# Kernel optimization log

Hardware: AMD Instinct MI355X
Metric: run time of the kernel (lower is better)

Reference implementation:

```python
import jax, jax.numpy as jnp
import numpy as np

B, S, D, H, HD = 2, 2048, 2048, 16, 128
SCALE = 1.0 / np.sqrt(HD)


def _rotate_half(x):
    x1, x2 = jnp.split(x, 2, axis=-1)
    return jnp.concatenate([-x2, x1], axis=-1)


def setup_inputs() -> dict:
    key = jax.random.key(0)
    ks = jax.random.split(key, 6)
    std = 0.02
    x = jax.random.normal(ks[0], (B, S, D), dtype=jnp.float32)
    Wq = jax.random.normal(ks[1], (D, D), dtype=jnp.float32) * std
    Wk = jax.random.normal(ks[2], (D, D), dtype=jnp.float32) * std
    Wv = jax.random.normal(ks[3], (D, D), dtype=jnp.float32) * std
    Wo = jax.random.normal(ks[4], (D, D), dtype=jnp.float32) * std
    # causal additive mask [1,1,S,S]
    neg = jnp.float32(-1e9)
    mask = jnp.where(jnp.tril(jnp.ones((S, S), dtype=bool)), 0.0, neg)[None, None]
    # standard RoPE tables [S, HD]
    inv_freq = 1.0 / (10000.0 ** (np.arange(0, HD, 2, dtype=np.float32) / HD))
    t = np.arange(S, dtype=np.float32)
    freqs = np.outer(t, inv_freq)                      # [S, HD/2]
    emb = np.concatenate([freqs, freqs], axis=-1)      # [S, HD]
    cos = jnp.asarray(np.cos(emb), dtype=jnp.float32)
    sin = jnp.asarray(np.sin(emb), dtype=jnp.float32)
    return {"x": x, "mask": mask, "cos": cos, "sin": sin,
            "Wq": Wq, "Wk": Wk, "Wv": Wv, "Wo": Wo}


def reference(x, mask, cos, sin, Wq, Wk, Wv, Wo):
    # projections (nn.Linear: y = x @ W.T)
    q = (x @ Wq.T).reshape(B, S, H, HD).transpose(0, 2, 1, 3)  # [B,H,S,HD]
    k = (x @ Wk.T).reshape(B, S, H, HD).transpose(0, 2, 1, 3)
    v = (x @ Wv.T).reshape(B, S, H, HD).transpose(0, 2, 1, 3)
    # inline RoPE
    c = cos[None, None]  # [1,1,S,HD]
    s = sin[None, None]
    q = q * c + _rotate_half(q) * s
    k = k * c + _rotate_half(k) * s
    # attention
    scores = jnp.einsum('bhqd,bhkd->bhqk', q, k) * SCALE + mask
    attn = jax.nn.softmax(scores, axis=-1)
    out = jnp.einsum('bhqk,bhkd->bhqd', attn, v)
    out = out.transpose(0, 2, 1, 3).reshape(B, S, D)
    return out @ Wo.T
```

## Files before the change

### kernel.cpp

```cpp
#include <hip/hip_runtime.h>
#include <hip/hip_bf16.h>
#include <type_traits>

#define B_  2
#define S_  2048
#define D_  2048
#define H_  16
#define HD_ 128
#define SCALE_ 0.08838834764831845f

using bf16 = __hip_bfloat16;
typedef __attribute__((ext_vector_type(8))) short short8;
typedef __attribute__((ext_vector_type(4))) short short4v;
typedef __attribute__((ext_vector_type(4))) float floatx4;

static __device__ __forceinline__ short bf16_bits(float f) {
    bf16 h = __float2bfloat16(f);
    short s;
    __builtin_memcpy(&s, &h, 2);
    return s;
}

static __device__ __forceinline__ void load_lds16(const bf16* gp, bf16* lp) {
    __builtin_amdgcn_global_load_lds(
        (const __attribute__((address_space(1))) void*)gp,
        (__attribute__((address_space(3))) void*)lp, 16, 0, 0);
}

__global__ __launch_bounds__(256) void conv_kernel(
        const float* s0, const float* s1, const float* s2,
        const float* s3, const float* s4, const float* s5,
        bf16* d0, bf16* d1, bf16* d2, bf16* d3, bf16* d4, bf16* d5) {
    int cid = blockIdx.x >> 12;
    int off = ((blockIdx.x & 4095) * 256 + threadIdx.x) * 4;
    const float* s; bf16* d;
    switch (cid) {
        case 0: s = s0; d = d0; break;
        case 1: s = s1; d = d1; break;
        case 2: s = s2; d = d2; break;
        case 3: s = s3; d = d3; break;
        case 4: s = s4; d = d4; break;
        default: s = s5; d = d5; break;
    }
    float4 f = *reinterpret_cast<const float4*>(s + off);
    short4v sv = {bf16_bits(f.x), bf16_bits(f.y), bf16_bits(f.z), bf16_bits(f.w)};
    *reinterpret_cast<short4v*>(d + off) = sv;
}

template <typename CT>
static __device__ __forceinline__ void gemm_core(const bf16* A, const bf16* W,
                                                 CT* C, int M, int N, int K,
                                                 int m0, int n0) {
    const int tid  = threadIdx.x;
    const int wave = tid >> 6;
    const int lane = tid & 63;
    const int wm = wave >> 1, wn = wave & 1;
    const int l16 = lane & 15, quad = lane >> 4;

    __shared__ __align__(16) bf16 As[128 * 32];
    __shared__ __align__(16) bf16 Bs[128 * 32];

    floatx4 acc[4][4];
    #pragma unroll
    for (int i = 0; i < 4; i++)
        #pragma unroll
        for (int j = 0; j < 4; j++)
            acc[i][j] = (floatx4){0.f, 0.f, 0.f, 0.f};

    const int srow = (lane >> 2);
    const int scol = (lane & 3) * 8;

    for (int kt = 0; kt < K; kt += 32) {
        #pragma unroll
        for (int i = 0; i < 2; i++) {
            int seg  = wave * 2 + i;
            int row  = seg * 16 + srow;
            load_lds16(&A[(size_t)(m0 + row) * K + kt + scol], &As[seg * 512]);
            load_lds16(&W[(size_t)(n0 + row) * K + kt + scol], &Bs[seg * 512]);
        }
        __syncthreads();

        short8 af[4], bfrag[4];
        #pragma unroll
        for (int m = 0; m < 4; m++)
            af[m] = *reinterpret_cast<const short8*>(&As[(wm * 64 + m * 16 + l16) * 32 + quad * 8]);
        #pragma unroll
        for (int n = 0; n < 4; n++)
            bfrag[n] = *reinterpret_cast<const short8*>(&Bs[(wn * 64 + n * 16 + l16) * 32 + quad * 8]);

        #pragma unroll
        for (int m = 0; m < 4; m++)
            #pragma unroll
            for (int n = 0; n < 4; n++)
                acc[m][n] = __builtin_amdgcn_mfma_f32_16x16x32_bf16(af[m], bfrag[n], acc[m][n], 0, 0, 0);
        __syncthreads();
    }

    #pragma unroll
    for (int m = 0; m < 4; m++) {
        #pragma unroll
        for (int n = 0; n < 4; n++) {
            #pragma unroll
            for (int r = 0; r < 4; r++) {
                int row = m0 + wm * 64 + m * 16 + quad * 4 + r;
                int col = n0 + wn * 64 + n * 16 + l16;
                if constexpr (std::is_same_v<CT, float>)
                    C[(size_t)row * N + col] = acc[m][n][r];
                else
                    C[(size_t)row * N + col] = __float2bfloat16(acc[m][n][r]);
            }
        }
    }
}

__global__ __launch_bounds__(256) void gemm_qkv(const bf16* __restrict__ X,
                                                const bf16* __restrict__ Wq,
                                                const bf16* __restrict__ Wk,
                                                const bf16* __restrict__ Wv,
                                                bf16* __restrict__ Q,
                                                bf16* __restrict__ Kb,
                                                bf16* __restrict__ V) {
    int wi = blockIdx.x >> 4;
    int n0 = (blockIdx.x & 15) * 128;
    int m0 = blockIdx.y * 128;
    const bf16* W = (wi == 0) ? Wq : (wi == 1) ? Wk : Wv;
    bf16* C = (wi == 0) ? Q : (wi == 1) ? Kb : V;
    gemm_core<bf16>(X, W, C, B_ * S_, D_, D_, m0, n0);
}

__global__ __launch_bounds__(256) void gemm_o(const bf16* __restrict__ A,
                                              const bf16* __restrict__ W,
                                              float* __restrict__ C) {
    gemm_core<float>(A, W, C, B_ * S_, D_, D_, blockIdx.y * 128, blockIdx.x * 128);
}

template <typename AT, typename CT>
__global__ __launch_bounds__(256) void gemm_bt(const AT* __restrict__ A,
                                               const float* __restrict__ W,
                                               CT* __restrict__ C,
                                               int M, int N, int K) {
    const int n0 = blockIdx.x * 128;
    const int m0 = blockIdx.y * 128;
    const int tid  = threadIdx.x;
    const int wave = tid >> 6;
    const int lane = tid & 63;
    const int wm = wave >> 1, wn = wave & 1;
    const int l16 = lane & 15, quad = lane >> 4;

    __shared__ __align__(16) bf16 As[128][40];
    __shared__ __align__(16) bf16 Bs[128][40];

    floatx4 acc[4][4];
    #pragma unroll
    for (int i = 0; i < 4; i++)
        #pragma unroll
        for (int j = 0; j < 4; j++)
            acc[i][j] = (floatx4){0.f, 0.f, 0.f, 0.f};

    for (int kt = 0; kt < K; kt += 32) {
        if constexpr (std::is_same_v<AT, float>) {
            #pragma unroll
            for (int i = 0; i < 4; i++) {
                int idx = i * 256 + tid;
                int row = idx >> 3;
                int ck  = idx & 7;
                float4 f = *reinterpret_cast<const float4*>(
                    &A[(size_t)(m0 + row) * K + kt + ck * 4]);
                short4v sv = {bf16_bits(f.x), bf16_bits(f.y),
                              bf16_bits(f.z), bf16_bits(f.w)};
                *reinterpret_cast<short4v*>(&As[row][ck * 4]) = sv;
            }
        } else {
            #pragma unroll
            for (int i = 0; i < 2; i++) {
                int idx = i * 256 + tid;
                int row = idx >> 2;
                int ck  = idx & 3;
                *reinterpret_cast<int4*>(&As[row][ck * 8]) =
                    *reinterpret_cast<const int4*>(
                        &A[(size_t)(m0 + row) * K + kt + ck * 8]);
            }
        }
        #pragma unroll
        for (int i = 0; i < 4; i++) {
            int idx = i * 256 + tid;
            int row = idx >> 3;
            int ck  = idx & 7;
            float4 f = *reinterpret_cast<const float4*>(
                &W[(size_t)(n0 + row) * K + kt + ck * 4]);
            short4v sv = {bf16_bits(f.x), bf16_bits(f.y),
                          bf16_bits(f.z), bf16_bits(f.w)};
            *reinterpret_cast<short4v*>(&Bs[row][ck * 4]) = sv;
        }
        __syncthreads();

        short8 af[4], bfrag[4];
        #pragma unroll
        for (int m = 0; m < 4; m++)
            af[m] = *reinterpret_cast<const short8*>(&As[wm * 64 + m * 16 + l16][quad * 8]);
        #pragma unroll
        for (int n = 0; n < 4; n++)
            bfrag[n] = *reinterpret_cast<const short8*>(&Bs[wn * 64 + n * 16 + l16][quad * 8]);

        #pragma unroll
        for (int m = 0; m < 4; m++)
            #pragma unroll
            for (int n = 0; n < 4; n++)
                acc[m][n] = __builtin_amdgcn_mfma_f32_16x16x32_bf16(af[m], bfrag[n], acc[m][n], 0, 0, 0);
        __syncthreads();
    }

    #pragma unroll
    for (int m = 0; m < 4; m++) {
        #pragma unroll
        for (int n = 0; n < 4; n++) {
            #pragma unroll
            for (int r = 0; r < 4; r++) {
                int row = m0 + wm * 64 + m * 16 + quad * 4 + r;
                int col = n0 + wn * 64 + n * 16 + l16;
                if constexpr (std::is_same_v<CT, float>)
                    C[(size_t)row * N + col] = acc[m][n][r];
                else
                    C[(size_t)row * N + col] = __float2bfloat16(acc[m][n][r]);
            }
        }
    }
}

__global__ __launch_bounds__(256) void rope_kernel(bf16* __restrict__ q,
                                                   bf16* __restrict__ k,
                                                   const float* __restrict__ cosT,
                                                   const float* __restrict__ sinT) {
    int idx = blockIdx.x * blockDim.x + threadIdx.x;
    int d = idx & 63;
    int h = (idx >> 6) & 15;
    int s = (idx >> 10) & 2047;
    int rest = idx >> 21;
    int b = rest & 1;
    bool isq = !(rest >> 1);
    bf16* p = isq ? q : k;
    float sc = isq ? SCALE_ : 1.0f;
    size_t base = ((size_t)(b * S_ + s)) * D_ + h * HD_;
    float v0 = __bfloat162float(p[base + d]);
    float v1 = __bfloat162float(p[base + d + 64]);
    float c0 = cosT[s * HD_ + d];
    float s0 = sinT[s * HD_ + d];
    float c1 = cosT[s * HD_ + d + 64];
    float s1 = sinT[s * HD_ + d + 64];
    p[base + d]      = __float2bfloat16((v0 * c0 - v1 * s0) * sc);
    p[base + d + 64] = __float2bfloat16((v1 * c1 + v0 * s1) * sc);
}

__global__ __launch_bounds__(256) void attn_kernel(const bf16* q,
                                                   const bf16* k,
                                                   const bf16* v,
                                                   bf16* o) {
    const int bx = blockIdx.x;
    const int qt = 15 - (bx & 15);
    const int h  = (bx >> 4) & 15;
    const int b  = bx >> 8;
    const int q0 = qt * 128;
    const int tid  = threadIdx.x;
    const int wave = tid >> 6;
    const int lane = tid & 63;
    const int l16 = lane & 15, quad = lane >> 4;

    __shared__ __align__(16) bf16  Ks[32][136];
    __shared__ __align__(16) short Vt[128][36];
    __shared__ __align__(16) short Pl[4][2][16][40];

    const size_t head_off = (size_t)b * S_ * D_ + (size_t)h * HD_;
    const bf16* qh = q + head_off;
    const bf16* kh = k + head_off;
    const short* vh = reinterpret_cast<const short*>(v) + head_off;

    short8 qf[2][4];
    #pragma unroll
    for (int mb = 0; mb < 2; mb++) {
        const bf16* qrow = qh + (size_t)(q0 + wave * 32 + mb * 16 + l16) * D_;
        #pragma unroll
        for (int dstep = 0; dstep < 4; dstep++)
            qf[mb][dstep] = *reinterpret_cast<const short8*>(qrow + dstep * 32 + quad * 8);
    }

    floatx4 ov[2][8];
    floatx4 lacc[2];
    #pragma unroll
    for (int mb = 0; mb < 2; mb++) {
        lacc[mb] = (floatx4){0.f, 0.f, 0.f, 0.f};
        #pragma unroll
        for (int i = 0; i < 8; i++) ov[mb][i] = (floatx4){0.f, 0.f, 0.f, 0.f};
    }
    float mrow[2][4];
    #pragma unroll
    for (int mb = 0; mb < 2; mb++)
        #pragma unroll
        for (int r = 0; r < 4; r++) mrow[mb][r] = -1e30f;

    const short ONEB = 0x3F80;
    const short8 ones = {ONEB, ONEB, ONEB, ONEB, ONEB, ONEB, ONEB, ONEB};

    const int vd  = tid & 127;
    const int vkh = tid >> 7;

    const int nkt = qt * 4 + 4;
    for (int kt = 0; kt < nkt; kt++) {
        const int k0 = kt * 32;
        #pragma unroll
        for (int i = 0; i < 2; i++) {
            int idx = i * 256 + tid;
            int row = idx >> 4;
            int ck  = idx & 15;
            *reinterpret_cast<int4*>(&Ks[row][ck * 8]) =
                *reinterpret_cast<const int4*>(kh + (size_t)(k0 + row) * D_ + ck * 8);
        }
        {
            const short* vcol = vh + (size_t)(k0 + vkh * 16) * D_ + vd;
            short tmp[16];
            #pragma unroll
            for (int r = 0; r < 16; r++)
                tmp[r] = vcol[(size_t)r * D_];
            #pragma unroll
            for (int c = 0; c < 4; c++) {
                short4v sv = {tmp[c*4], tmp[c*4+1], tmp[c*4+2], tmp[c*4+3]};
                *reinterpret_cast<short4v*>(&Vt[vd][vkh * 16 + c * 4]) = sv;
            }
        }
        __syncthreads();

        floatx4 sc[2][2];
        #pragma unroll
        for (int mb = 0; mb < 2; mb++)
            #pragma unroll
            for (int nb = 0; nb < 2; nb++)
                sc[mb][nb] = (floatx4){0.f, 0.f, 0.f, 0.f};
        #pragma unroll
        for (int dstep = 0; dstep < 4; dstep++) {
            short8 kf0 = *reinterpret_cast<const short8*>(&Ks[l16][dstep * 32 + quad * 8]);
            short8 kf1 = *reinterpret_cast<const short8*>(&Ks[16 + l16][dstep * 32 + quad * 8]);
            #pragma unroll
            for (int mb = 0; mb < 2; mb++) {
                sc[mb][0] = __builtin_amdgcn_mfma_f32_16x16x32_bf16(qf[mb][dstep], kf0, sc[mb][0], 0, 0, 0);
                sc[mb][1] = __builtin_amdgcn_mfma_f32_16x16x32_bf16(qf[mb][dstep], kf1, sc[mb][1], 0, 0, 0);
            }
        }

        #pragma unroll
        for (int mb = 0; mb < 2; mb++) {
            const int qbase = q0 + wave * 32 + mb * 16;
            const bool need_mask = (k0 + 31 > qbase);
            #pragma unroll
            for (int r = 0; r < 4; r++) {
                float s0 = sc[mb][0][r];
                float s1 = sc[mb][1][r];
                if (need_mask) {
                    int qg = qbase + quad * 4 + r;
                    if (k0 + l16 > qg)      s0 = -1e30f;
                    if (k0 + 16 + l16 > qg) s1 = -1e30f;
                }
                float mx = fmaxf(s0, s1);
                #pragma unroll
                for (int off = 1; off < 16; off <<= 1)
                    mx = fmaxf(mx, __shfl_xor(mx, off, 16));
                float mnew  = fmaxf(mrow[mb][r], mx);
                float alpha = __expf(mrow[mb][r] - mnew);
                mrow[mb][r] = mnew;
                Pl[wave][mb][quad * 4 + r][l16]      = bf16_bits(__expf(s0 - mnew));
                Pl[wave][mb][quad * 4 + r][16 + l16] = bf16_bits(__expf(s1 - mnew));
                lacc[mb][r] *= alpha;
                #pragma unroll
                for (int db = 0; db < 8; db++) ov[mb][db][r] *= alpha;
            }
        }

        __asm__ volatile("s_waitcnt lgkmcnt(0)" ::: "memory");

        short8 pf0 = *reinterpret_cast<const short8*>(&Pl[wave][0][l16][quad * 8]);
        short8 pf1 = *reinterpret_cast<const short8*>(&Pl[wave][1][l16][quad * 8]);
        #pragma unroll
        for (int db = 0; db < 8; db++) {
            const short* vp = &Vt[db * 16 + l16][quad * 8];
            short4v a = *reinterpret_cast<const short4v*>(vp);
            short4v c = *reinterpret_cast<const short4v*>(vp + 4);
            short8 vf = {a[0], a[1], a[2], a[3], c[0], c[1], c[2], c[3]};
            ov[0][db] = __builtin_amdgcn_mfma_f32_16x16x32_bf16(pf0, vf, ov[0][db], 0, 0, 0);
            ov[1][db] = __builtin_amdgcn_mfma_f32_16x16x32_bf16(pf1, vf, ov[1][db], 0, 0, 0);
        }
        lacc[0] = __builtin_amdgcn_mfma_f32_16x16x32_bf16(pf0, ones, lacc[0], 0, 0, 0);
        lacc[1] = __builtin_amdgcn_mfma_f32_16x16x32_bf16(pf1, ones, lacc[1], 0, 0, 0);
        __syncthreads();
    }

    bf16* oh = o + head_off;
    #pragma unroll
    for (int mb = 0; mb < 2; mb++) {
        #pragma unroll
        for (int r = 0; r < 4; r++) {
            float inv = 1.f / lacc[mb][r];
            int srow = q0 + wave * 32 + mb * 16 + quad * 4 + r;
            #pragma unroll
            for (int db = 0; db < 8; db++)
                oh[(size_t)srow * D_ + db * 16 + l16] = __float2bfloat16(ov[mb][db][r] * inv);
        }
    }
}

extern "C" void kernel_launch(void* const* d_in, const int* in_sizes, int n_in,
                              void* d_out, int out_size, void* d_ws, size_t ws_size,
                              hipStream_t stream) {
    const float* x    = (const float*)d_in[0];
    const float* cosT = (const float*)d_in[2];
    const float* sinT = (const float*)d_in[3];
    const float* Wq   = (const float*)d_in[4];
    const float* Wk   = (const float*)d_in[5];
    const float* Wv   = (const float*)d_in[6];
    const float* Wo   = (const float*)d_in[7];
    float* out = (float*)d_out;

    const size_t tsz = (size_t)B_ * S_ * D_;
    const size_t wsz = (size_t)D_ * D_;
    bf16* qb = (bf16*)d_ws;
    bf16* kb = qb + tsz;
    bf16* vb = kb + tsz;
    bf16* ab = qb;

    const size_t need = (3 * tsz + tsz + 4 * wsz) * sizeof(bf16);

    if (ws_size >= need) {
        bf16* xb  = vb + tsz;
        bf16* wqb = xb + tsz;
        bf16* wkb = wqb + wsz;
        bf16* wvb = wkb + wsz;
        bf16* wob = wvb + wsz;

        conv_kernel<<<24576, 256, 0, stream>>>(
            x, x + wsz, Wq, Wk, Wv, Wo,
            xb, xb + wsz, wqb, wkb, wvb, wob);

        gemm_qkv<<<dim3(48, 32), 256, 0, stream>>>(xb, wqb, wkb, wvb, qb, kb, vb);

        rope_kernel<<<(2 * B_ * S_ * H_ * 64) / 256, 256, 0, stream>>>(qb, kb, cosT, sinT);

        attn_kernel<<<B_ * H_ * (S_ / 128), 256, 0, stream>>>(qb, kb, vb, ab);

        gemm_o<<<dim3(16, 32), 256, 0, stream>>>(ab, wob, out);
    } else {
        dim3 ggrid(D_ / 128, (B_ * S_) / 128);
        gemm_bt<float, bf16><<<ggrid, 256, 0, stream>>>(x, Wq, qb, B_ * S_, D_, D_);
        gemm_bt<float, bf16><<<ggrid, 256, 0, stream>>>(x, Wk, kb, B_ * S_, D_, D_);
        gemm_bt<float, bf16><<<ggrid, 256, 0, stream>>>(x, Wv, vb, B_ * S_, D_, D_);

        rope_kernel<<<(2 * B_ * S_ * H_ * 64) / 256, 256, 0, stream>>>(qb, kb, cosT, sinT);

        attn_kernel<<<B_ * H_ * (S_ / 128), 256, 0, stream>>>(qb, kb, vb, ab);

        gemm_bt<bf16, float><<<ggrid, 256, 0, stream>>>(ab, Wo, out, B_ * S_, D_, D_);
    }
}
```

Before: 503.3 us.

## Widen attention key tile to 64, use exp2 softmax with lazy rescaling

The attention kernel now processes 64 keys per iteration instead of 32, halving the number of loop iterations and block-wide barriers and issuing more MFMAs per loaded tile. The softmax switches to exp2 by folding log2(e) into the Q scale inside the RoPE kernel. It also skips the running-max update and output rescale when no row's tile maximum exceeds the stored max by more than 8 (in log2 units). Costs are higher LDS usage and register pressure, and probabilities can reach up to 2^8 before normalisation, which adds some bf16 rounding risk.

```diff
diff --git a/kernel.cpp b/kernel.cpp
--- a/kernel.cpp
+++ b/kernel.cpp
@@ -8,6 +8,7 @@
 #define H_  16
 #define HD_ 128
 #define SCALE_ 0.08838834764831845f
+#define LOG2E_ 1.44269504088896340736f
 
 using bf16 = __hip_bfloat16;
 typedef __attribute__((ext_vector_type(8))) short short8;
@@ -239,7 +240,7 @@
     int b = rest & 1;
     bool isq = !(rest >> 1);
     bf16* p = isq ? q : k;
-    float sc = isq ? SCALE_ : 1.0f;
+    float sc = isq ? (SCALE_ * LOG2E_) : 1.0f;
     size_t base = ((size_t)(b * S_ + s)) * D_ + h * HD_;
     float v0 = __bfloat162float(p[base + d]);
     float v1 = __bfloat162float(p[base + d + 64]);
@@ -265,9 +266,9 @@
     const int lane = tid & 63;
     const int l16 = lane & 15, quad = lane >> 4;
 
-    __shared__ __align__(16) bf16  Ks[32][136];
-    __shared__ __align__(16) short Vt[128][36];
-    __shared__ __align__(16) short Pl[4][2][16][40];
+    __shared__ __align__(16) bf16  Ks[64][136];
+    __shared__ __align__(16) short Vt[128][72];
+    __shared__ __align__(16) short Pl[4][2][16][72];
 
     const size_t head_off = (size_t)b * S_ * D_ + (size_t)h * HD_;
     const bf16* qh = q + head_off;
@@ -303,19 +304,20 @@
     const int vd  = tid & 127;
     const int vkh = tid >> 7;
 
-    const int nkt = qt * 4 + 4;
+    const int nkt = qt * 2 + 2;
     for (int kt = 0; kt < nkt; kt++) {
-        const int k0 = kt * 32;
-        #pragma unroll
-        for (int i = 0; i < 2; i++) {
+        const int k0 = kt * 64;
+        #pragma unroll
+        for (int i = 0; i < 4; i++) {
             int idx = i * 256 + tid;
             int row = idx >> 4;
             int ck  = idx & 15;
             *reinterpret_cast<int4*>(&Ks[row][ck * 8]) =
                 *reinterpret_cast<const int4*>(kh + (size_t)(k0 + row) * D_ + ck * 8);
         }
-        {
-            const short* vcol = vh + (size_t)(k0 + vkh * 16) * D_ + vd;
+        #pragma unroll
+        for (int g = 0; g < 2; g++) {
+            const short* vcol = vh + (size_t)(k0 + g * 32 + vkh * 16) * D_ + vd;
             short tmp[16];
             #pragma unroll
             for (int r = 0; r < 16; r++)
@@ -323,71 +325,106 @@
             #pragma unroll
             for (int c = 0; c < 4; c++) {
                 short4v sv = {tmp[c*4], tmp[c*4+1], tmp[c*4+2], tmp[c*4+3]};
-                *reinterpret_cast<short4v*>(&Vt[vd][vkh * 16 + c * 4]) = sv;
-            }
-        }
-        __syncthreads();
-
-        floatx4 sc[2][2];
+                *reinterpret_cast<short4v*>(&Vt[vd][g * 32 + vkh * 16 + c * 4]) = sv;
+            }
+        }
+        __syncthreads();
+
+        floatx4 sc[2][4];
         #pragma unroll
         for (int mb = 0; mb < 2; mb++)
             #pragma unroll
-            for (int nb = 0; nb < 2; nb++)
+            for (int nb = 0; nb < 4; nb++)
                 sc[mb][nb] = (floatx4){0.f, 0.f, 0.f, 0.f};
         #pragma unroll
         for (int dstep = 0; dstep < 4; dstep++) {
-            short8 kf0 = *reinterpret_cast<const short8*>(&Ks[l16][dstep * 32 + quad * 8]);
-            short8 kf1 = *reinterpret_cast<const short8*>(&Ks[16 + l16][dstep * 32 + quad * 8]);
-            #pragma unroll
-            for (int mb = 0; mb < 2; mb++) {
-                sc[mb][0] = __builtin_amdgcn_mfma_f32_16x16x32_bf16(qf[mb][dstep], kf0, sc[mb][0], 0, 0, 0);
-                sc[mb][1] = __builtin_amdgcn_mfma_f32_16x16x32_bf16(qf[mb][dstep], kf1, sc[mb][1], 0, 0, 0);
-            }
-        }
-
+            short8 kf[4];
+            #pragma unroll
+            for (int nb = 0; nb < 4; nb++)
+                kf[nb] = *reinterpret_cast<const short8*>(&Ks[nb * 16 + l16][dstep * 32 + quad * 8]);
+            #pragma unroll
+            for (int mb = 0; mb < 2; mb++)
+                #pragma unroll
+                for (int nb = 0; nb < 4; nb++)
+                    sc[mb][nb] = __builtin_amdgcn_mfma_f32_16x16x32_bf16(qf[mb][dstep], kf[nb], sc[mb][nb], 0, 0, 0);
+        }
+
+        float tmax[2][4];
         #pragma unroll
         for (int mb = 0; mb < 2; mb++) {
             const int qbase = q0 + wave * 32 + mb * 16;
-            const bool need_mask = (k0 + 31 > qbase);
+            const bool need_mask = (k0 + 63 > qbase);
             #pragma unroll
             for (int r = 0; r < 4; r++) {
-                float s0 = sc[mb][0][r];
-                float s1 = sc[mb][1][r];
                 if (need_mask) {
                     int qg = qbase + quad * 4 + r;
-                    if (k0 + l16 > qg)      s0 = -1e30f;
-                    if (k0 + 16 + l16 > qg) s1 = -1e30f;
+                    #pragma unroll
+                    for (int nb = 0; nb < 4; nb++)
+                        if (k0 + nb * 16 + l16 > qg) sc[mb][nb][r] = -1e30f;
                 }
-                float mx = fmaxf(s0, s1);
+                float mx = fmaxf(fmaxf(sc[mb][0][r], sc[mb][1][r]),
+                                 fmaxf(sc[mb][2][r], sc[mb][3][r]));
                 #pragma unroll
                 for (int off = 1; off < 16; off <<= 1)
                     mx = fmaxf(mx, __shfl_xor(mx, off, 16));
-                float mnew  = fmaxf(mrow[mb][r], mx);
-                float alpha = __expf(mrow[mb][r] - mnew);
-                mrow[mb][r] = mnew;
-                Pl[wave][mb][quad * 4 + r][l16]      = bf16_bits(__expf(s0 - mnew));
-                Pl[wave][mb][quad * 4 + r][16 + l16] = bf16_bits(__expf(s1 - mnew));
-                lacc[mb][r] *= alpha;
+                tmax[mb][r] = mx;
+            }
+        }
+
+        bool ok = true;
+        #pragma unroll
+        for (int mb = 0; mb < 2; mb++)
+            #pragma unroll
+            for (int r = 0; r < 4; r++)
+                ok &= (tmax[mb][r] <= mrow[mb][r] + 8.0f);
+        if (!__all(ok)) {
+            #pragma unroll
+            for (int mb = 0; mb < 2; mb++) {
                 #pragma unroll
-                for (int db = 0; db < 8; db++) ov[mb][db][r] *= alpha;
-            }
-        }
+                for (int r = 0; r < 4; r++) {
+                    float mnew  = fmaxf(mrow[mb][r], tmax[mb][r]);
+                    float alpha = exp2f(mrow[mb][r] - mnew);
+                    mrow[mb][r] = mnew;
+                    lacc[mb][r] *= alpha;
+                    #pragma unroll
+                    for (int db = 0; db < 8; db++) ov[mb][db][r] *= alpha;
+                }
+            }
+        }
+
+        #pragma unroll
+        for (int mb = 0; mb < 2; mb++)
+            #pragma unroll
+            for (int r = 0; r < 4; r++) {
+                float m = mrow[mb][r];
+                #pragma unroll
+                for (int nb = 0; nb < 4; nb++)
+                    Pl[wave][mb][quad * 4 + r][nb * 16 + l16] =
+                        bf16_bits(exp2f(sc[mb][nb][r] - m));
+            }
 
         __asm__ volatile("s_waitcnt lgkmcnt(0)" ::: "memory");
 
-        short8 pf0 = *reinterpret_cast<const short8*>(&Pl[wave][0][l16][quad * 8]);
-        short8 pf1 = *reinterpret_cast<const short8*>(&Pl[wave][1][l16][quad * 8]);
+        short8 pf[2][2];
+        #pragma unroll
+        for (int mb = 0; mb < 2; mb++)
+            #pragma unroll
+            for (int ks = 0; ks < 2; ks++)
+                pf[mb][ks] = *reinterpret_cast<const short8*>(&Pl[wave][mb][l16][ks * 32 + quad * 8]);
         #pragma unroll
         for (int db = 0; db < 8; db++) {
-            const short* vp = &Vt[db * 16 + l16][quad * 8];
-            short4v a = *reinterpret_cast<const short4v*>(vp);
-            short4v c = *reinterpret_cast<const short4v*>(vp + 4);
-            short8 vf = {a[0], a[1], a[2], a[3], c[0], c[1], c[2], c[3]};
-            ov[0][db] = __builtin_amdgcn_mfma_f32_16x16x32_bf16(pf0, vf, ov[0][db], 0, 0, 0);
-            ov[1][db] = __builtin_amdgcn_mfma_f32_16x16x32_bf16(pf1, vf, ov[1][db], 0, 0, 0);
-        }
-        lacc[0] = __builtin_amdgcn_mfma_f32_16x16x32_bf16(pf0, ones, lacc[0], 0, 0, 0);
-        lacc[1] = __builtin_amdgcn_mfma_f32_16x16x32_bf16(pf1, ones, lacc[1], 0, 0, 0);
+            #pragma unroll
+            for (int ks = 0; ks < 2; ks++) {
+                short8 vf = *reinterpret_cast<const short8*>(&Vt[db * 16 + l16][ks * 32 + quad * 8]);
+                ov[0][db] = __builtin_amdgcn_mfma_f32_16x16x32_bf16(pf[0][ks], vf, ov[0][db], 0, 0, 0);
+                ov[1][db] = __builtin_amdgcn_mfma_f32_16x16x32_bf16(pf[1][ks], vf, ov[1][db], 0, 0, 0);
+            }
+        }
+        #pragma unroll
+        for (int mb = 0; mb < 2; mb++) {
+            lacc[mb] = __builtin_amdgcn_mfma_f32_16x16x32_bf16(pf[mb][0], ones, lacc[mb], 0, 0, 0);
+            lacc[mb] = __builtin_amdgcn_mfma_f32_16x16x32_bf16(pf[mb][1], ones, lacc[mb], 0, 0, 0);
+        }
         __syncthreads();
     }
 
```

Result: slower. 577.6 us (+14.8%).

## Prefetch K/V tiles into registers and use lazy exp2 softmax rescaling

Applied to the files above, without the earlier changes.

The attention loop now loads the next K/V tile from global memory into registers while the current tile is being computed, which hides load latency behind the MFMA work. The softmax switches to exp2 by folding log2(e) into the Q scaling inside the RoPE kernel. Rescaling of the running max and accumulators is skipped when every row's new max stays within 8 (log2 units) of the stored max, using a wave-wide vote. This costs extra registers for the prefetch and allows unnormalized P values up to 256, which could affect bf16 precision.

```diff
diff --git a/kernel.cpp b/kernel.cpp
--- a/kernel.cpp
+++ b/kernel.cpp
@@ -8,6 +8,7 @@
 #define H_  16
 #define HD_ 128
 #define SCALE_ 0.08838834764831845f
+#define LOG2E_ 1.44269504088896340736f
 
 using bf16 = __hip_bfloat16;
 typedef __attribute__((ext_vector_type(8))) short short8;
@@ -239,7 +240,7 @@
     int b = rest & 1;
     bool isq = !(rest >> 1);
     bf16* p = isq ? q : k;
-    float sc = isq ? SCALE_ : 1.0f;
+    float sc = isq ? (SCALE_ * LOG2E_) : 1.0f;
     size_t base = ((size_t)(b * S_ + s)) * D_ + h * HD_;
     float v0 = __bfloat162float(p[base + d]);
     float v1 = __bfloat162float(p[base + d + 64]);
@@ -303,30 +304,43 @@
     const int vd  = tid & 127;
     const int vkh = tid >> 7;
 
+    const int krow0 = tid >> 4;
+    const int kck   = (tid & 15) * 8;
+
+    int4 kreg[2];
+    short vreg[16];
+
+    {
+        kreg[0] = *reinterpret_cast<const int4*>(kh + (size_t)krow0 * D_ + kck);
+        kreg[1] = *reinterpret_cast<const int4*>(kh + (size_t)(16 + krow0) * D_ + kck);
+        const short* vcol = vh + (size_t)(vkh * 16) * D_ + vd;
+        #pragma unroll
+        for (int r = 0; r < 16; r++)
+            vreg[r] = vcol[(size_t)r * D_];
+    }
+
     const int nkt = qt * 4 + 4;
     for (int kt = 0; kt < nkt; kt++) {
         const int k0 = kt * 32;
-        #pragma unroll
-        for (int i = 0; i < 2; i++) {
-            int idx = i * 256 + tid;
-            int row = idx >> 4;
-            int ck  = idx & 15;
-            *reinterpret_cast<int4*>(&Ks[row][ck * 8]) =
-                *reinterpret_cast<const int4*>(kh + (size_t)(k0 + row) * D_ + ck * 8);
-        }
-        {
-            const short* vcol = vh + (size_t)(k0 + vkh * 16) * D_ + vd;
-            short tmp[16];
+
+        *reinterpret_cast<int4*>(&Ks[krow0][kck]) = kreg[0];
+        *reinterpret_cast<int4*>(&Ks[16 + krow0][kck]) = kreg[1];
+        #pragma unroll
+        for (int c = 0; c < 4; c++) {
+            short4v sv = {vreg[c*4], vreg[c*4+1], vreg[c*4+2], vreg[c*4+3]};
+            *reinterpret_cast<short4v*>(&Vt[vd][vkh * 16 + c * 4]) = sv;
+        }
+        __syncthreads();
+
+        if (kt + 1 < nkt) {
+            const int k0n = k0 + 32;
+            kreg[0] = *reinterpret_cast<const int4*>(kh + (size_t)(k0n + krow0) * D_ + kck);
+            kreg[1] = *reinterpret_cast<const int4*>(kh + (size_t)(k0n + 16 + krow0) * D_ + kck);
+            const short* vcol = vh + (size_t)(k0n + vkh * 16) * D_ + vd;
             #pragma unroll
             for (int r = 0; r < 16; r++)
-                tmp[r] = vcol[(size_t)r * D_];
-            #pragma unroll
-            for (int c = 0; c < 4; c++) {
-                short4v sv = {tmp[c*4], tmp[c*4+1], tmp[c*4+2], tmp[c*4+3]};
-                *reinterpret_cast<short4v*>(&Vt[vd][vkh * 16 + c * 4]) = sv;
-            }
-        }
-        __syncthreads();
+                vreg[r] = vcol[(size_t)r * D_];
+        }
 
         floatx4 sc[2][2];
         #pragma unroll
@@ -345,33 +359,55 @@
             }
         }
 
+        float tmax[2][4];
         #pragma unroll
         for (int mb = 0; mb < 2; mb++) {
             const int qbase = q0 + wave * 32 + mb * 16;
             const bool need_mask = (k0 + 31 > qbase);
             #pragma unroll
             for (int r = 0; r < 4; r++) {
-                float s0 = sc[mb][0][r];
-                float s1 = sc[mb][1][r];
                 if (need_mask) {
                     int qg = qbase + quad * 4 + r;
-                    if (k0 + l16 > qg)      s0 = -1e30f;
-                    if (k0 + 16 + l16 > qg) s1 = -1e30f;
+                    if (k0 + l16 > qg)      sc[mb][0][r] = -1e30f;
+                    if (k0 + 16 + l16 > qg) sc[mb][1][r] = -1e30f;
                 }
-                float mx = fmaxf(s0, s1);
+                float mx = fmaxf(sc[mb][0][r], sc[mb][1][r]);
                 #pragma unroll
                 for (int off = 1; off < 16; off <<= 1)
                     mx = fmaxf(mx, __shfl_xor(mx, off, 16));
-                float mnew  = fmaxf(mrow[mb][r], mx);
-                float alpha = __expf(mrow[mb][r] - mnew);
-                mrow[mb][r] = mnew;
-                Pl[wave][mb][quad * 4 + r][l16]      = bf16_bits(__expf(s0 - mnew));
-                Pl[wave][mb][quad * 4 + r][16 + l16] = bf16_bits(__expf(s1 - mnew));
-                lacc[mb][r] *= alpha;
+                tmax[mb][r] = mx;
+            }
+        }
+
+        bool ok = true;
+        #pragma unroll
+        for (int mb = 0; mb < 2; mb++)
+            #pragma unroll
+            for (int r = 0; r < 4; r++)
+                ok &= (tmax[mb][r] <= mrow[mb][r] + 8.0f);
+        if (!__all(ok)) {
+            #pragma unroll
+            for (int mb = 0; mb < 2; mb++) {
                 #pragma unroll
-                for (int db = 0; db < 8; db++) ov[mb][db][r] *= alpha;
-            }
-        }
+                for (int r = 0; r < 4; r++) {
+                    float mnew  = fmaxf(mrow[mb][r], tmax[mb][r]);
+                    float alpha = exp2f(mrow[mb][r] - mnew);
+                    mrow[mb][r] = mnew;
+                    lacc[mb][r] *= alpha;
+                    #pragma unroll
+                    for (int db = 0; db < 8; db++) ov[mb][db][r] *= alpha;
+                }
+            }
+        }
+
+        #pragma unroll
+        for (int mb = 0; mb < 2; mb++)
+            #pragma unroll
+            for (int r = 0; r < 4; r++) {
+                float m = mrow[mb][r];
+                Pl[wave][mb][quad * 4 + r][l16]      = bf16_bits(exp2f(sc[mb][0][r] - m));
+                Pl[wave][mb][quad * 4 + r][16 + l16] = bf16_bits(exp2f(sc[mb][1][r] - m));
+            }
 
         __asm__ volatile("s_waitcnt lgkmcnt(0)" ::: "memory");
 
```

Result: slower. 678.3 us (+34.8%).
